# Kernel tuning notes

Hardware: AMD Instinct MI355X
Metric: run time of the kernel (lower is better)

The kernel has to match this reference:

```python
import jax, jax.numpy as jnp
import numpy as np

N = 100000   # nodes
E = 800000   # edges
G = 512      # graphs in batch
F_IN = 75    # num_features_xd


def setup_inputs() -> dict:
    key = jax.random.key(0)
    ks = jax.random.split(key, 12)
    s = 0.05
    x = jax.random.normal(ks[0], (N, F_IN), jnp.float32)
    edge_index = jax.random.randint(ks[1], (2, E), 0, N, dtype=jnp.int32)
    # deterministic near-equal graph assignment (sorted, no empty graphs)
    batch = ((jnp.arange(N) * G) // N).astype(jnp.int32)
    W1 = jax.random.normal(ks[2], (F_IN, F_IN), jnp.float32) * s
    b1 = jnp.zeros((F_IN,), jnp.float32)
    W2 = jax.random.normal(ks[3], (F_IN, 2 * F_IN), jnp.float32) * s
    b2 = jnp.zeros((2 * F_IN,), jnp.float32)
    W3 = jax.random.normal(ks[4], (2 * F_IN, 4 * F_IN), jnp.float32) * s
    b3 = jnp.zeros((4 * F_IN,), jnp.float32)
    Wg1 = jax.random.normal(ks[5], (4 * F_IN, 1024), jnp.float32) * s
    bg1 = jnp.zeros((1024,), jnp.float32)
    Wg2 = jax.random.normal(ks[6], (1024, 128), jnp.float32) * s
    bg2 = jnp.zeros((128,), jnp.float32)
    return {"x": x, "edge_index": edge_index, "batch": batch,
            "W1": W1, "b1": b1, "W2": W2, "b2": b2, "W3": W3, "b3": b3,
            "Wg1": Wg1, "bg1": bg1, "Wg2": Wg2, "bg2": bg2}


def reference(x, edge_index, batch, W1, b1, W2, b2, W3, b3, Wg1, bg1, Wg2, bg2):
    n = x.shape[0]
    row, col = edge_index[0], edge_index[1]
    loop = jnp.arange(n, dtype=row.dtype)
    row_f = jnp.concatenate([row, loop])  # source (with self loops)
    col_f = jnp.concatenate([col, loop])  # target
    # symmetric GCN normalization: deg from targets incl. self loops
    deg = jax.ops.segment_sum(jnp.ones_like(col_f, dtype=x.dtype), col_f, num_segments=n)
    dinv = jnp.where(deg > 0, deg ** -0.5, 0.0)
    norm = dinv[row_f] * dinv[col_f]  # [E+N]

    def gcn(h, W, b):
        h = h @ W  # transform first (PyG GCNConv order)
        msg = norm[:, None] * h[row_f]  # gather + scale
        return jax.ops.segment_sum(msg, col_f, num_segments=n) + b

    h = jax.nn.relu(gcn(x, W1, b1))
    h = jax.nn.relu(gcn(h, W2, b2))
    h = jax.nn.relu(gcn(h, W3, b3))
    g = jax.ops.segment_max(h, batch, num_segments=G)  # global max pool -> [G, 300]
    g = jax.nn.relu(g @ Wg1 + bg1)
    # dropout is identity at inference
    return g @ Wg2 + bg2  # [G, 128]
```

## Files before the change

kernel.cpp:

```cpp
#include <hip/hip_runtime.h>

typedef __attribute__((ext_vector_type(8))) short short8v;
typedef __attribute__((ext_vector_type(4))) float f32x4;
typedef unsigned short u16;

__device__ inline u16 f2bf(float x){
  union{float f; unsigned u;} v; v.f = x;
  unsigned r = (v.u + 0x7FFFu + ((v.u >> 16) & 1u)) >> 16;
  return (u16)r;
}
__device__ inline float b2f(u16 u){
  union{unsigned u32; float f;} w; w.u32 = (unsigned)u << 16; return w.f;
}


__global__ void k_deg(const int* __restrict__ col, int* __restrict__ indeg, int E){
  int e = blockIdx.x*blockDim.x + threadIdx.x;
  if (e < E) atomicAdd(&indeg[col[e]], 1);
}

__global__ void k_dinv(const int* __restrict__ indeg, float* __restrict__ dinv, int n){
  int i = blockIdx.x*blockDim.x + threadIdx.x;
  if (i < n) dinv[i] = rsqrtf((float)(indeg[i] + 1));
}

__global__ __launch_bounds__(256) void k_scan1(const int* __restrict__ indeg, int* __restrict__ rp,
                                               int* __restrict__ bsums, int n){
  __shared__ int s[256];
  int b = blockIdx.x, t = threadIdx.x;
  int base = b*1024 + t*4;
  int v[4]; int tsum = 0;
  #pragma unroll
  for (int j=0;j<4;j++){ v[j] = (base+j < n) ? indeg[base+j] : 0; tsum += v[j]; }
  s[t] = tsum; __syncthreads();
  for (int d=1; d<256; d<<=1){ int x = (t>=d) ? s[t-d] : 0; __syncthreads(); s[t] += x; __syncthreads(); }
  int run = s[t] - tsum;
  if (t == 255) bsums[b] = s[255];
  #pragma unroll
  for (int j=0;j<4;j++){ if (base+j < n){ rp[base+j] = run; } run += v[j]; }
}

__global__ __launch_bounds__(128) void k_scan2(int* bsums, int* rp, int nb, int n){
  __shared__ int s[128];
  int t = threadIdx.x;
  int orig = (t < nb) ? bsums[t] : 0;
  s[t] = orig; __syncthreads();
  for (int d=1; d<128; d<<=1){ int x = (t>=d) ? s[t-d] : 0; __syncthreads(); s[t] += x; __syncthreads(); }
  if (t < nb) bsums[t] = s[t] - orig;
  if (t == 127) rp[n] = s[127];
}

__global__ void k_scan3(int* __restrict__ rp, int* __restrict__ nxt, const int* __restrict__ bsums, int n){
  int i = blockIdx.x*blockDim.x + threadIdx.x;
  if (i < n){ int v = rp[i] + bsums[i >> 10]; rp[i] = v; nxt[i] = v; }
}

__global__ void k_scatter(const int* __restrict__ row, const int* __restrict__ col,
                          int* __restrict__ nxt, int* __restrict__ csr, int E){
  int e = blockIdx.x*blockDim.x + threadIdx.x;
  if (e < E){ int c = col[e]; int p = atomicAdd(&nxt[c], 1); csr[p] = row[e]; }
}

__global__ void k_padb(const float* __restrict__ x, u16* __restrict__ xb, int n){
  long total = (long)n*80;
  for (long idx = blockIdx.x*(long)blockDim.x + threadIdx.x; idx < total; idx += (long)gridDim.x*blockDim.x){
    int r = (int)(idx/80), fcol = (int)(idx%80);
    xb[idx] = f2bf(fcol < 75 ? x[(size_t)r*75 + fcol] : 0.f);
  }
}

__global__ void k_wt(const float* __restrict__ W, u16* __restrict__ Wt,
                     int Kreal, int NC, int KPAD, int NCP){
  int idx = blockIdx.x*blockDim.x + threadIdx.x;
  if (idx >= NCP*KPAD) return;
  int c = idx / KPAD, k = idx % KPAD;
  float v = (c < NC && k < Kreal) ? W[(size_t)k*NC + c] : 0.0f;
  Wt[idx] = f2bf(v);
}


template<int FP>
__global__ __launch_bounds__(256) void k_prop_bf(const u16* __restrict__ h, const float* __restrict__ dinv,
                                                 const int* __restrict__ rp, const int* __restrict__ csr,
                                                 u16* __restrict__ out, int n){
  constexpr int TPN = FP/8;
  constexpr int NPB = 256/TPN;
  int q = threadIdx.x / TPN;
  int t = threadIdx.x - q*TPN;
  if (q >= NPB) return;
  int node = blockIdx.x*NPB + q;
  if (node >= n) return;
  int f = 8*t;
  float di = dinv[node];
  float acc[8];
  {
    short8v v = *(const short8v*)&h[(size_t)node*FP + f];
    #pragma unroll
    for (int i=0;i<8;i++) acc[i] = di*b2f((u16)v[i]);
  }
  int e0 = rp[node], e1 = rp[node+1];
  int e = e0;
  for (; e + 4 <= e1; e += 4){
    int s0 = csr[e], s1 = csr[e+1], s2 = csr[e+2], s3 = csr[e+3];
    float d0 = dinv[s0], d1 = dinv[s1], d2 = dinv[s2], d3 = dinv[s3];
    short8v v0 = *(const short8v*)&h[(size_t)s0*FP + f];
    short8v v1 = *(const short8v*)&h[(size_t)s1*FP + f];
    short8v v2 = *(const short8v*)&h[(size_t)s2*FP + f];
    short8v v3 = *(const short8v*)&h[(size_t)s3*FP + f];
    #pragma unroll
    for (int i=0;i<8;i++)
      acc[i] += d0*b2f((u16)v0[i]) + d1*b2f((u16)v1[i]) + d2*b2f((u16)v2[i]) + d3*b2f((u16)v3[i]);
  }
  for (; e < e1; ++e){
    int s = csr[e]; float ds = dinv[s];
    short8v v = *(const short8v*)&h[(size_t)s*FP + f];
    #pragma unroll
    for (int i=0;i<8;i++) acc[i] += ds*b2f((u16)v[i]);
  }
  short8v o;
  #pragma unroll
  for (int i=0;i<8;i++) o[i] = (short)f2bf(di*acc[i]);
  *(short8v*)&out[(size_t)node*FP + f] = o;
}


template<int KPAD, int LDA, int POOL>
__global__ __launch_bounds__(256) void k_gemm_bf(
    const u16* __restrict__ A, const u16* __restrict__ Wt,
    const float* __restrict__ bias,
    u16* __restrict__ out, int ldout, int NC, int NT,
    const int* __restrict__ batch, unsigned* __restrict__ gpool, int ldg,
    int n, int G)
{
  constexpr int SA = KPAD + 8;
  constexpr int SW = KPAD + 8;
  constexpr int C8 = KPAD/8;
  constexpr int R8 = LDA/8;
  __shared__ u16 As[128*SA];
  __shared__ u16 Ws[64*SW];
  __shared__ unsigned pmax[2][64];

  int tid = threadIdx.x;
  int r0 = blockIdx.x * 128;
  int w = tid >> 6, l = tid & 63;

  #pragma unroll
  for (int i = 0; i < 128*C8/256; ++i){
    int idx = tid + 256*i;
    int r = idx / C8, c8 = idx % C8;
    short8v v = (short8v){0,0,0,0,0,0,0,0};
    if (r0 + r < n && c8 < R8) v = *(const short8v*)&A[(size_t)(r0+r)*LDA + 8*c8];
    *(short8v*)&As[r*SA + 8*c8] = v;
  }

  const u16* Ab = &As[(32*w + (l & 15))*SA + (l >> 4)*8];
  const u16* Bb = &Ws[(l & 15)*SW + (l >> 4)*8];

  for (int ct = 0; ct < NT; ++ct){
    if (ct) __syncthreads();
    #pragma unroll
    for (int i = 0; i < 64*C8/256; ++i){
      int idx = tid + 256*i;
      int wr = idx / C8, wk = idx % C8;
      *(short8v*)&Ws[wr*SW + 8*wk] = *(const short8v*)&Wt[(size_t)(ct*64 + wr)*KPAD + 8*wk];
    }
    if (POOL){ if (tid < 128) pmax[tid>>6][tid&63] = 0u; }
    __syncthreads();

    f32x4 acc[2][4];
    #pragma unroll
    for (int a=0;a<2;a++)
      #pragma unroll
      for (int b=0;b<4;b++) acc[a][b] = (f32x4){0.f,0.f,0.f,0.f};

    #pragma unroll
    for (int ks = 0; ks < KPAD/32; ++ks){
      short8v a0 = *(const short8v*)(Ab + ks*32);
      short8v a1 = *(const short8v*)(Ab + 16*SA + ks*32);
      short8v b0 = *(const short8v*)(Bb + ks*32);
      short8v b1 = *(const short8v*)(Bb + 16*SW + ks*32);
      short8v b2 = *(const short8v*)(Bb + 32*SW + ks*32);
      short8v b3 = *(const short8v*)(Bb + 48*SW + ks*32);
      acc[0][0] = __builtin_amdgcn_mfma_f32_16x16x32_bf16(a0, b0, acc[0][0], 0, 0, 0);
      acc[0][1] = __builtin_amdgcn_mfma_f32_16x16x32_bf16(a0, b1, acc[0][1], 0, 0, 0);
      acc[0][2] = __builtin_amdgcn_mfma_f32_16x16x32_bf16(a0, b2, acc[0][2], 0, 0, 0);
      acc[0][3] = __builtin_amdgcn_mfma_f32_16x16x32_bf16(a0, b3, acc[0][3], 0, 0, 0);
      acc[1][0] = __builtin_amdgcn_mfma_f32_16x16x32_bf16(a1, b0, acc[1][0], 0, 0, 0);
      acc[1][1] = __builtin_amdgcn_mfma_f32_16x16x32_bf16(a1, b1, acc[1][1], 0, 0, 0);
      acc[1][2] = __builtin_amdgcn_mfma_f32_16x16x32_bf16(a1, b2, acc[1][2], 0, 0, 0);
      acc[1][3] = __builtin_amdgcn_mfma_f32_16x16x32_bf16(a1, b3, acc[1][3], 0, 0, 0);
    }

    int cbase = ct*64;
    if (!POOL){
      #pragma unroll
      for (int rf=0;rf<2;rf++){
        int rbase = r0 + 32*w + 16*rf + 4*(l >> 4);
        #pragma unroll
        for (int cf=0;cf<4;cf++){
          int c = cbase + 16*cf + (l & 15);
          if (c >= ldout) continue;
          float bv = (c < NC) ? bias[c] : 0.f;
          #pragma unroll
          for (int r=0;r<4;r++){
            int rr = rbase + r;
            if (rr < n){
              float v = (c < NC) ? fmaxf(acc[rf][cf][r] + bv, 0.f) : 0.f;
              out[(size_t)rr*ldout + c] = f2bf(v);
            }
          }
        }
      }
    } else {
      int g0 = batch[r0];
      #pragma unroll
      for (int rf=0;rf<2;rf++){
        int rbase = r0 + 32*w + 16*rf + 4*(l >> 4);
        #pragma unroll
        for (int cf=0;cf<4;cf++){
          int c = cbase + 16*cf + (l & 15);
          if (c >= NC) continue;
          float bv = bias[c];
          int curgi = -1; float m = 0.f;
          #pragma unroll
          for (int r=0;r<4;r++){
            int rr = rbase + r;
            if (rr < n){
              int gi = batch[rr] - g0; if (gi > 1) gi = 1;
              float v = fmaxf(acc[rf][cf][r] + bv, 0.f);
              if (gi != curgi){
                if (curgi >= 0 && m > 0.f) atomicMax(&pmax[curgi][16*cf + (l&15)], __float_as_uint(m));
                curgi = gi; m = v;
              } else m = fmaxf(m, v);
            }
          }
          if (curgi >= 0 && m > 0.f) atomicMax(&pmax[curgi][16*cf + (l&15)], __float_as_uint(m));
        }
      }
      __syncthreads();
      if (tid < 128){
        int gi = tid >> 6, cc = tid & 63;
        unsigned v = pmax[gi][cc];
        int gg = g0 + gi;
        if (v != 0u && (cbase + cc) < NC && gg < G)
          atomicMax(&gpool[(size_t)gg*ldg + (cbase + cc)], v);
      }
    }
  }
}


__global__ __launch_bounds__(256) void k_gemm_kloop(
    const float* __restrict__ A, int lda, int Ktot,
    const u16* __restrict__ Wt, int ldw,
    const float* __restrict__ bias,
    float* __restrict__ out, int ldout, int NC,
    int n, int relu)
{
  constexpr int SA = 72, SW = 72;
  __shared__ u16 As[128*SA];
  __shared__ u16 Ws[64*SW];
  int tid = threadIdx.x;
  int r0 = blockIdx.x * 128, c0 = blockIdx.y * 64;
  int w = tid >> 6, l = tid & 63;

  f32x4 acc[2][4];
  #pragma unroll
  for (int a=0;a<2;a++)
    #pragma unroll
    for (int b=0;b<4;b++) acc[a][b] = (f32x4){0.f,0.f,0.f,0.f};

  const u16* Ab = &As[(32*w + (l & 15))*SA + (l >> 4)*8];
  const u16* Bb = &Ws[(l & 15)*SW + (l >> 4)*8];

  for (int k0 = 0; k0 < Ktot; k0 += 64){
    #pragma unroll
    for (int i=0;i<8;i++){
      int idx = tid + 256*i;
      int r = idx >> 4, c4 = idx & 15;
      float4 v = make_float4(0.f,0.f,0.f,0.f);
      if (r0 + r < n) v = *(const float4*)&A[(size_t)(r0+r)*lda + k0 + 4*c4];
      unsigned p01 = (unsigned)f2bf(v.x) | ((unsigned)f2bf(v.y) << 16);
      unsigned p23 = (unsigned)f2bf(v.z) | ((unsigned)f2bf(v.w) << 16);
      *(uint2*)&As[r*SA + 4*c4] = make_uint2(p01, p23);
    }
    #pragma unroll
    for (int i=0;i<2;i++){
      int idx = tid + 256*i;
      int wr = idx >> 3, wk = idx & 7;
      short8v wv = *(const short8v*)&Wt[(size_t)(c0+wr)*ldw + k0 + 8*wk];
      *(short8v*)&Ws[wr*SW + 8*wk] = wv;
    }
    __syncthreads();
    #pragma unroll
    for (int ks = 0; ks < 2; ++ks){
      short8v a0 = *(const short8v*)(Ab + ks*32);
      short8v a1 = *(const short8v*)(Ab + 16*SA + ks*32);
      short8v b0 = *(const short8v*)(Bb + ks*32);
      short8v b1 = *(const short8v*)(Bb + 16*SW + ks*32);
      short8v b2 = *(const short8v*)(Bb + 32*SW + ks*32);
      short8v b3 = *(const short8v*)(Bb + 48*SW + ks*32);
      acc[0][0] = __builtin_amdgcn_mfma_f32_16x16x32_bf16(a0, b0, acc[0][0], 0, 0, 0);
      acc[0][1] = __builtin_amdgcn_mfma_f32_16x16x32_bf16(a0, b1, acc[0][1], 0, 0, 0);
      acc[0][2] = __builtin_amdgcn_mfma_f32_16x16x32_bf16(a0, b2, acc[0][2], 0, 0, 0);
      acc[0][3] = __builtin_amdgcn_mfma_f32_16x16x32_bf16(a0, b3, acc[0][3], 0, 0, 0);
      acc[1][0] = __builtin_amdgcn_mfma_f32_16x16x32_bf16(a1, b0, acc[1][0], 0, 0, 0);
      acc[1][1] = __builtin_amdgcn_mfma_f32_16x16x32_bf16(a1, b1, acc[1][1], 0, 0, 0);
      acc[1][2] = __builtin_amdgcn_mfma_f32_16x16x32_bf16(a1, b2, acc[1][2], 0, 0, 0);
      acc[1][3] = __builtin_amdgcn_mfma_f32_16x16x32_bf16(a1, b3, acc[1][3], 0, 0, 0);
    }
    __syncthreads();
  }

  #pragma unroll
  for (int rf=0;rf<2;rf++){
    int rbase = r0 + 32*w + 16*rf + 4*(l >> 4);
    #pragma unroll
    for (int cf=0;cf<4;cf++){
      int c = c0 + 16*cf + (l & 15);
      if (c >= NC) continue;
      float bv = bias[c];
      #pragma unroll
      for (int r=0;r<4;r++){
        int rr = rbase + r;
        if (rr < n){
          float v = acc[rf][cf][r] + bv;
          if (relu) v = fmaxf(v, 0.f);
          out[(size_t)rr*ldout + c] = v;
        }
      }
    }
  }
}


extern "C" void kernel_launch(void* const* d_in, const int* in_sizes, int n_in,
                              void* d_out, int out_size, void* d_ws, size_t ws_size,
                              hipStream_t stream)
{
  const float* x   = (const float*)d_in[0];
  const int*   ei  = (const int*)d_in[1];
  const int*   batch = (const int*)d_in[2];
  const float* W1  = (const float*)d_in[3]; const float* b1  = (const float*)d_in[4];
  const float* W2  = (const float*)d_in[5]; const float* b2  = (const float*)d_in[6];
  const float* W3  = (const float*)d_in[7]; const float* b3  = (const float*)d_in[8];
  const float* Wg1 = (const float*)d_in[9]; const float* bg1 = (const float*)d_in[10];
  const float* Wg2 = (const float*)d_in[11]; const float* bg2 = (const float*)d_in[12];
  float* out = (float*)d_out;

  const int F1 = 75;
  int n = in_sizes[0] / F1;
  int E = in_sizes[1] / 2;
  int G = out_size / 128;
  const int* row = ei;
  const int* col = ei + E;

  char* ws = (char*)d_ws;
  size_t off = 0;
  auto alloc = [&](size_t bytes){ size_t o = off; off += (bytes + 255) & ~(size_t)255; return o; };
  u16*   xb    = (u16*)  (ws + alloc((size_t)n*80*2));
  u16*   qb    = (u16*)  (ws + alloc((size_t)n*160*2));
  u16*   h2b   = (u16*)  (ws + alloc((size_t)n*160*2));
  float* dinv  = (float*)(ws + alloc((size_t)n*4));
  int*   indeg = (int*)  (ws + alloc((size_t)n*4));
  int*   rp    = (int*)  (ws + alloc((size_t)(n+1)*4));
  int*   nxt   = (int*)  (ws + alloc((size_t)n*4));
  int*   csr   = (int*)  (ws + alloc((size_t)E*4));
  int*   bsums = (int*)  (ws + alloc(1024*4));
  unsigned* g  = (unsigned*)(ws + alloc((size_t)G*320*4));
  float* gh    = (float*)(ws + alloc((size_t)G*1024*4));
  u16* Wt1  = (u16*)(ws + alloc((size_t)128*96*2));
  u16* Wt2  = (u16*)(ws + alloc((size_t)192*96*2));
  u16* Wt3  = (u16*)(ws + alloc((size_t)320*160*2));
  u16* Wg1t = (u16*)(ws + alloc((size_t)1024*320*2));
  u16* Wg2t = (u16*)(ws + alloc((size_t)128*1024*2));
  u16* h1b = xb;

  hipMemsetAsync(indeg, 0, (size_t)n*4, stream);
  hipMemsetAsync(g, 0, (size_t)G*320*4, stream);

  k_deg<<<(E+255)/256, 256, 0, stream>>>(col, indeg, E);
  k_dinv<<<(n+255)/256, 256, 0, stream>>>(indeg, dinv, n);

  int nb = (n + 1023) / 1024;
  k_scan1<<<nb, 256, 0, stream>>>(indeg, rp, bsums, n);
  k_scan2<<<1, 128, 0, stream>>>(bsums, rp, nb, n);
  k_scan3<<<(n+255)/256, 256, 0, stream>>>(rp, nxt, bsums, n);
  k_scatter<<<(E+255)/256, 256, 0, stream>>>(row, col, nxt, csr, E);

  k_padb<<<4096, 256, 0, stream>>>(x, xb, n);
  k_wt<<<(128*96+255)/256, 256, 0, stream>>>(W1, Wt1, 75, 75, 96, 128);
  k_wt<<<(192*96+255)/256, 256, 0, stream>>>(W2, Wt2, 75, 150, 96, 192);
  k_wt<<<(320*160+255)/256, 256, 0, stream>>>(W3, Wt3, 150, 300, 160, 320);
  k_wt<<<(1024*320+255)/256, 256, 0, stream>>>(Wg1, Wg1t, 300, 1024, 320, 1024);
  k_wt<<<(128*1024+255)/256, 256, 0, stream>>>(Wg2, Wg2t, 1024, 128, 1024, 128);

  int mb = (n + 127) / 128;

  k_prop_bf<80><<<(n+24)/25, 256, 0, stream>>>(xb, dinv, rp, csr, qb, n);
  k_gemm_bf<96,80,0><<<mb, 256, 0, stream>>>(qb, Wt1, b1, h1b, 80, 75, 2,
                                             nullptr, nullptr, 0, n, G);
  k_prop_bf<80><<<(n+24)/25, 256, 0, stream>>>(h1b, dinv, rp, csr, qb, n);
  k_gemm_bf<96,80,0><<<mb, 256, 0, stream>>>(qb, Wt2, b2, h2b, 160, 150, 3,
                                             nullptr, nullptr, 0, n, G);
  k_prop_bf<160><<<(n+11)/12, 256, 0, stream>>>(h2b, dinv, rp, csr, qb, n);
  k_gemm_bf<160,160,1><<<mb, 256, 0, stream>>>(qb, Wt3, b3, nullptr, 0, 300, 5,
                                               batch, g, 320, n, G);
  {
    dim3 grid(G/128, 1024/64);
    k_gemm_kloop<<<grid, 256, 0, stream>>>((const float*)g, 320, 320, Wg1t, 320, bg1,
                                           gh, 1024, 1024, G, 1);
  }
  {
    dim3 grid(G/128, 128/64);
    k_gemm_kloop<<<grid, 256, 0, stream>>>(gh, 1024, 1024, Wg2t, 1024, bg2,
                                           out, 128, 128, G, 0);
  }
}
```

Baseline: 497.3 us.

## Store node features in feature-major 8-column slabs for propagation and GEMM

Node feature buffers switch from row-major to a feature-major layout: separate slabs of 8 bf16 columns across all nodes. Each propagation block now handles one 8-feature slab for 256 nodes, so the gathered working set per pass is 16 bytes per node and should stay cache-resident. The GEMM reads and writes slabs, and its row tile drops from 128 to 64 to keep occupancy up. The cost is more redundant CSR/dinv traversal (once per slab), less A-fragment reuse per wave in the GEMM, and scattered 2-byte output stores.

```diff
diff --git a/kernel.cpp b/kernel.cpp
--- a/kernel.cpp
+++ b/kernel.cpp
@@ -61,11 +61,17 @@
   if (e < E){ int c = col[e]; int p = atomicAdd(&nxt[c], 1); csr[p] = row[e]; }
 }
 
-__global__ void k_padb(const float* __restrict__ x, u16* __restrict__ xb, int n){
-  long total = (long)n*80;
+__global__ void k_padfm(const float* __restrict__ x, u16* __restrict__ xfm, int n){
+  long total = 10L*n;
   for (long idx = blockIdx.x*(long)blockDim.x + threadIdx.x; idx < total; idx += (long)gridDim.x*blockDim.x){
-    int r = (int)(idx/80), fcol = (int)(idx%80);
-    xb[idx] = f2bf(fcol < 75 ? x[(size_t)r*75 + fcol] : 0.f);
+    int c8 = (int)(idx / n); int node = (int)(idx - (long)c8*n);
+    short8v o;
+    #pragma unroll
+    for (int j=0;j<8;j++){
+      int f = 8*c8 + j;
+      o[j] = (short)f2bf(f < 75 ? x[(size_t)node*75 + f] : 0.f);
+    }
+    *(short8v*)&xfm[idx*8] = o;
   }
 }
 
@@ -79,22 +85,20 @@
 }
 
 
-template<int FP>
-__global__ __launch_bounds__(256) void k_prop_bf(const u16* __restrict__ h, const float* __restrict__ dinv,
-                                                 const int* __restrict__ rp, const int* __restrict__ csr,
-                                                 u16* __restrict__ out, int n){
-  constexpr int TPN = FP/8;
-  constexpr int NPB = 256/TPN;
-  int q = threadIdx.x / TPN;
-  int t = threadIdx.x - q*TPN;
-  if (q >= NPB) return;
-  int node = blockIdx.x*NPB + q;
+__global__ __launch_bounds__(256) void k_prop_fm(
+    const u16* __restrict__ h, const float* __restrict__ dinv,
+    const int* __restrict__ rp, const int* __restrict__ csr,
+    u16* __restrict__ out, int n, int nblk)
+{
+  int c8 = blockIdx.x / nblk;
+  int node = (blockIdx.x - c8*nblk)*256 + threadIdx.x;
   if (node >= n) return;
-  int f = 8*t;
+  const u16* __restrict__ slab = h + (size_t)c8*n*8;
+  u16* __restrict__ oslab = out + (size_t)c8*n*8;
   float di = dinv[node];
   float acc[8];
   {
-    short8v v = *(const short8v*)&h[(size_t)node*FP + f];
+    short8v v = *(const short8v*)&slab[(size_t)node*8];
     #pragma unroll
     for (int i=0;i<8;i++) acc[i] = di*b2f((u16)v[i]);
   }
@@ -103,57 +107,57 @@
   for (; e + 4 <= e1; e += 4){
     int s0 = csr[e], s1 = csr[e+1], s2 = csr[e+2], s3 = csr[e+3];
     float d0 = dinv[s0], d1 = dinv[s1], d2 = dinv[s2], d3 = dinv[s3];
-    short8v v0 = *(const short8v*)&h[(size_t)s0*FP + f];
-    short8v v1 = *(const short8v*)&h[(size_t)s1*FP + f];
-    short8v v2 = *(const short8v*)&h[(size_t)s2*FP + f];
-    short8v v3 = *(const short8v*)&h[(size_t)s3*FP + f];
+    short8v v0 = *(const short8v*)&slab[(size_t)s0*8];
+    short8v v1 = *(const short8v*)&slab[(size_t)s1*8];
+    short8v v2 = *(const short8v*)&slab[(size_t)s2*8];
+    short8v v3 = *(const short8v*)&slab[(size_t)s3*8];
     #pragma unroll
     for (int i=0;i<8;i++)
       acc[i] += d0*b2f((u16)v0[i]) + d1*b2f((u16)v1[i]) + d2*b2f((u16)v2[i]) + d3*b2f((u16)v3[i]);
   }
   for (; e < e1; ++e){
     int s = csr[e]; float ds = dinv[s];
-    short8v v = *(const short8v*)&h[(size_t)s*FP + f];
+    short8v v = *(const short8v*)&slab[(size_t)s*8];
     #pragma unroll
     for (int i=0;i<8;i++) acc[i] += ds*b2f((u16)v[i]);
   }
   short8v o;
   #pragma unroll
   for (int i=0;i<8;i++) o[i] = (short)f2bf(di*acc[i]);
-  *(short8v*)&out[(size_t)node*FP + f] = o;
-}
-
-
-template<int KPAD, int LDA, int POOL>
-__global__ __launch_bounds__(256) void k_gemm_bf(
-    const u16* __restrict__ A, const u16* __restrict__ Wt,
+  *(short8v*)&oslab[(size_t)node*8] = o;
+}
+
+
+template<int KPAD, int FPIN, int POOL>
+__global__ __launch_bounds__(256) void k_gemm_fm(
+    const u16* __restrict__ Afm, const u16* __restrict__ Wt,
     const float* __restrict__ bias,
-    u16* __restrict__ out, int ldout, int NC, int NT,
+    u16* __restrict__ outfm, int NC, int FPOUT, int NT,
     const int* __restrict__ batch, unsigned* __restrict__ gpool, int ldg,
     int n, int G)
 {
   constexpr int SA = KPAD + 8;
   constexpr int SW = KPAD + 8;
   constexpr int C8 = KPAD/8;
-  constexpr int R8 = LDA/8;
-  __shared__ u16 As[128*SA];
+  constexpr int R8 = FPIN/8;
+  __shared__ u16 As[64*SA];
   __shared__ u16 Ws[64*SW];
   __shared__ unsigned pmax[2][64];
 
   int tid = threadIdx.x;
-  int r0 = blockIdx.x * 128;
+  int r0 = blockIdx.x * 64;
   int w = tid >> 6, l = tid & 63;
 
   #pragma unroll
-  for (int i = 0; i < 128*C8/256; ++i){
+  for (int i = 0; i < 64*C8/256; ++i){
     int idx = tid + 256*i;
-    int r = idx / C8, c8 = idx % C8;
+    int r = idx & 63, c8 = idx >> 6;
     short8v v = (short8v){0,0,0,0,0,0,0,0};
-    if (r0 + r < n && c8 < R8) v = *(const short8v*)&A[(size_t)(r0+r)*LDA + 8*c8];
+    if (c8 < R8 && r0 + r < n) v = *(const short8v*)&Afm[((size_t)c8*n + r0 + r)*8];
     *(short8v*)&As[r*SA + 8*c8] = v;
   }
 
-  const u16* Ab = &As[(32*w + (l & 15))*SA + (l >> 4)*8];
+  const u16* Ab = &As[(16*w + (l & 15))*SA + (l >> 4)*8];
   const u16* Bb = &Ws[(l & 15)*SW + (l >> 4)*8];
 
   for (int ct = 0; ct < NT; ++ct){
@@ -167,75 +171,63 @@
     if (POOL){ if (tid < 128) pmax[tid>>6][tid&63] = 0u; }
     __syncthreads();
 
-    f32x4 acc[2][4];
-    #pragma unroll
-    for (int a=0;a<2;a++)
-      #pragma unroll
-      for (int b=0;b<4;b++) acc[a][b] = (f32x4){0.f,0.f,0.f,0.f};
+    f32x4 acc[4];
+    #pragma unroll
+    for (int b=0;b<4;b++) acc[b] = (f32x4){0.f,0.f,0.f,0.f};
 
     #pragma unroll
     for (int ks = 0; ks < KPAD/32; ++ks){
       short8v a0 = *(const short8v*)(Ab + ks*32);
-      short8v a1 = *(const short8v*)(Ab + 16*SA + ks*32);
       short8v b0 = *(const short8v*)(Bb + ks*32);
       short8v b1 = *(const short8v*)(Bb + 16*SW + ks*32);
       short8v b2 = *(const short8v*)(Bb + 32*SW + ks*32);
       short8v b3 = *(const short8v*)(Bb + 48*SW + ks*32);
-      acc[0][0] = __builtin_amdgcn_mfma_f32_16x16x32_bf16(a0, b0, acc[0][0], 0, 0, 0);
-      acc[0][1] = __builtin_amdgcn_mfma_f32_16x16x32_bf16(a0, b1, acc[0][1], 0, 0, 0);
-      acc[0][2] = __builtin_amdgcn_mfma_f32_16x16x32_bf16(a0, b2, acc[0][2], 0, 0, 0);
-      acc[0][3] = __builtin_amdgcn_mfma_f32_16x16x32_bf16(a0, b3, acc[0][3], 0, 0, 0);
-      acc[1][0] = __builtin_amdgcn_mfma_f32_16x16x32_bf16(a1, b0, acc[1][0], 0, 0, 0);
-      acc[1][1] = __builtin_amdgcn_mfma_f32_16x16x32_bf16(a1, b1, acc[1][1], 0, 0, 0);
-      acc[1][2] = __builtin_amdgcn_mfma_f32_16x16x32_bf16(a1, b2, acc[1][2], 0, 0, 0);
-      acc[1][3] = __builtin_amdgcn_mfma_f32_16x16x32_bf16(a1, b3, acc[1][3], 0, 0, 0);
-    }
-
+      acc[0] = __builtin_amdgcn_mfma_f32_16x16x32_bf16(a0, b0, acc[0], 0, 0, 0);
+      acc[1] = __builtin_amdgcn_mfma_f32_16x16x32_bf16(a0, b1, acc[1], 0, 0, 0);
+      acc[2] = __builtin_amdgcn_mfma_f32_16x16x32_bf16(a0, b2, acc[2], 0, 0, 0);
+      acc[3] = __builtin_amdgcn_mfma_f32_16x16x32_bf16(a0, b3, acc[3], 0, 0, 0);
+    }
+
+    int rbase = r0 + 16*w + 4*(l >> 4);
     int cbase = ct*64;
     if (!POOL){
       #pragma unroll
-      for (int rf=0;rf<2;rf++){
-        int rbase = r0 + 32*w + 16*rf + 4*(l >> 4);
+      for (int cf=0;cf<4;cf++){
+        int c = cbase + 16*cf + (l & 15);
+        if (c >= FPOUT) continue;
+        bool real = (c < NC);
+        float bv = real ? bias[c] : 0.f;
+        size_t obase = ((size_t)(c >> 3)*n)*8 + (c & 7);
         #pragma unroll
-        for (int cf=0;cf<4;cf++){
-          int c = cbase + 16*cf + (l & 15);
-          if (c >= ldout) continue;
-          float bv = (c < NC) ? bias[c] : 0.f;
-          #pragma unroll
-          for (int r=0;r<4;r++){
-            int rr = rbase + r;
-            if (rr < n){
-              float v = (c < NC) ? fmaxf(acc[rf][cf][r] + bv, 0.f) : 0.f;
-              out[(size_t)rr*ldout + c] = f2bf(v);
-            }
+        for (int r=0;r<4;r++){
+          int rr = rbase + r;
+          if (rr < n){
+            float v = real ? fmaxf(acc[cf][r] + bv, 0.f) : 0.f;
+            outfm[obase + (size_t)rr*8] = f2bf(v);
           }
         }
       }
     } else {
       int g0 = batch[r0];
       #pragma unroll
-      for (int rf=0;rf<2;rf++){
-        int rbase = r0 + 32*w + 16*rf + 4*(l >> 4);
+      for (int cf=0;cf<4;cf++){
+        int c = cbase + 16*cf + (l & 15);
+        if (c >= NC) continue;
+        float bv = bias[c];
+        int curgi = -1; float m = 0.f;
         #pragma unroll
-        for (int cf=0;cf<4;cf++){
-          int c = cbase + 16*cf + (l & 15);
-          if (c >= NC) continue;
-          float bv = bias[c];
-          int curgi = -1; float m = 0.f;
-          #pragma unroll
-          for (int r=0;r<4;r++){
-            int rr = rbase + r;
-            if (rr < n){
-              int gi = batch[rr] - g0; if (gi > 1) gi = 1;
-              float v = fmaxf(acc[rf][cf][r] + bv, 0.f);
-              if (gi != curgi){
-                if (curgi >= 0 && m > 0.f) atomicMax(&pmax[curgi][16*cf + (l&15)], __float_as_uint(m));
-                curgi = gi; m = v;
-              } else m = fmaxf(m, v);
-            }
+        for (int r=0;r<4;r++){
+          int rr = rbase + r;
+          if (rr < n){
+            int gi = batch[rr] - g0; if (gi > 1) gi = 1;
+            float v = fmaxf(acc[cf][r] + bv, 0.f);
+            if (gi != curgi){
+              if (curgi >= 0 && m > 0.f) atomicMax(&pmax[curgi][16*cf + (l&15)], __float_as_uint(m));
+              curgi = gi; m = v;
+            } else m = fmaxf(m, v);
           }
-          if (curgi >= 0 && m > 0.f) atomicMax(&pmax[curgi][16*cf + (l&15)], __float_as_uint(m));
         }
+        if (curgi >= 0 && m > 0.f) atomicMax(&pmax[curgi][16*cf + (l&15)], __float_as_uint(m));
       }
       __syncthreads();
       if (tid < 128){
@@ -358,9 +350,9 @@
   char* ws = (char*)d_ws;
   size_t off = 0;
   auto alloc = [&](size_t bytes){ size_t o = off; off += (bytes + 255) & ~(size_t)255; return o; };
-  u16*   xb    = (u16*)  (ws + alloc((size_t)n*80*2));
-  u16*   qb    = (u16*)  (ws + alloc((size_t)n*160*2));
-  u16*   h2b   = (u16*)  (ws + alloc((size_t)n*160*2));
+  u16*   xfm   = (u16*)  (ws + alloc((size_t)n*80*2));
+  u16*   qfm   = (u16*)  (ws + alloc((size_t)n*160*2));
+  u16*   h2fm  = (u16*)  (ws + alloc((size_t)n*160*2));
   float* dinv  = (float*)(ws + alloc((size_t)n*4));
   int*   indeg = (int*)  (ws + alloc((size_t)n*4));
   int*   rp    = (int*)  (ws + alloc((size_t)(n+1)*4));
@@ -374,7 +366,7 @@
   u16* Wt3  = (u16*)(ws + alloc((size_t)320*160*2));
   u16* Wg1t = (u16*)(ws + alloc((size_t)1024*320*2));
   u16* Wg2t = (u16*)(ws + alloc((size_t)128*1024*2));
-  u16* h1b = xb;
+  u16* h1fm = xfm;
 
   hipMemsetAsync(indeg, 0, (size_t)n*4, stream);
   hipMemsetAsync(g, 0, (size_t)G*320*4, stream);
@@ -388,24 +380,25 @@
   k_scan3<<<(n+255)/256, 256, 0, stream>>>(rp, nxt, bsums, n);
   k_scatter<<<(E+255)/256, 256, 0, stream>>>(row, col, nxt, csr, E);
 
-  k_padb<<<4096, 256, 0, stream>>>(x, xb, n);
+  k_padfm<<<2048, 256, 0, stream>>>(x, xfm, n);
   k_wt<<<(128*96+255)/256, 256, 0, stream>>>(W1, Wt1, 75, 75, 96, 128);
   k_wt<<<(192*96+255)/256, 256, 0, stream>>>(W2, Wt2, 75, 150, 96, 192);
   k_wt<<<(320*160+255)/256, 256, 0, stream>>>(W3, Wt3, 150, 300, 160, 320);
   k_wt<<<(1024*320+255)/256, 256, 0, stream>>>(Wg1, Wg1t, 300, 1024, 320, 1024);
   k_wt<<<(128*1024+255)/256, 256, 0, stream>>>(Wg2, Wg2t, 1024, 128, 1024, 128);
 
-  int mb = (n + 127) / 128;
-
-  k_prop_bf<80><<<(n+24)/25, 256, 0, stream>>>(xb, dinv, rp, csr, qb, n);
-  k_gemm_bf<96,80,0><<<mb, 256, 0, stream>>>(qb, Wt1, b1, h1b, 80, 75, 2,
-                                             nullptr, nullptr, 0, n, G);
-  k_prop_bf<80><<<(n+24)/25, 256, 0, stream>>>(h1b, dinv, rp, csr, qb, n);
-  k_gemm_bf<96,80,0><<<mb, 256, 0, stream>>>(qb, Wt2, b2, h2b, 160, 150, 3,
-                                             nullptr, nullptr, 0, n, G);
-  k_prop_bf<160><<<(n+11)/12, 256, 0, stream>>>(h2b, dinv, rp, csr, qb, n);
-  k_gemm_bf<160,160,1><<<mb, 256, 0, stream>>>(qb, Wt3, b3, nullptr, 0, 300, 5,
-                                               batch, g, 320, n, G);
+  int nblk = (n + 255) / 256;
+  int mb64 = (n + 63) / 64;
+
+  k_prop_fm<<<10*nblk, 256, 0, stream>>>(xfm, dinv, rp, csr, qfm, n, nblk);
+  k_gemm_fm<96,80,0><<<mb64, 256, 0, stream>>>(qfm, Wt1, b1, h1fm, 75, 80, 2,
+                                               nullptr, nullptr, 0, n, G);
+  k_prop_fm<<<10*nblk, 256, 0, stream>>>(h1fm, dinv, rp, csr, qfm, n, nblk);
+  k_gemm_fm<96,80,0><<<mb64, 256, 0, stream>>>(qfm, Wt2, b2, h2fm, 150, 160, 3,
+                                               nullptr, nullptr, 0, n, G);
+  k_prop_fm<<<20*nblk, 256, 0, stream>>>(h2fm, dinv, rp, csr, qfm, n, nblk);
+  k_gemm_fm<160,160,1><<<mb64, 256, 0, stream>>>(qfm, Wt3, b3, nullptr, 300, 320, 5,
+                                                 batch, g, 320, n, G);
   {
     dim3 grid(G/128, 1024/64);
     k_gemm_kloop<<<grid, 256, 0, stream>>>((const float*)g, 320, 320, Wg1t, 320, bg1,
```

New measurement: 768.3 us. +54.5%, slower.
